# Optimization experiments

Hardware: AMD Instinct MI355X
Metric: run time of the kernel (lower is better)

Reference implementation:

```python
import jax, jax.numpy as jnp
import numpy as np

TAU = 0.1  # temperature (registered buffer, non-trainable)
EPS = 1e-12  # F.normalize eps


def setup_inputs() -> dict:
    key = jax.random.key(0)
    k1, k2 = jax.random.split(key)
    B, C = 4096, 512
    z1 = jax.random.normal(k1, (B, C), dtype=jnp.float32)
    z2 = jax.random.normal(k2, (B, C), dtype=jnp.float32)
    return {"z1": z1, "z2": z2}


def _l2_normalize(x):
    # matches F.normalize(p=2, dim=1): x / max(||x||, eps)
    n = jnp.sqrt(jnp.sum(x * x, axis=1, keepdims=True))
    return x / jnp.maximum(n, EPS)


def reference(z1, z2):
    B = z1.shape[0]
    N = 2 * B
    z = jnp.concatenate([_l2_normalize(z1), _l2_normalize(z2)], axis=0)  # [2B, C]
    # cosine similarity of unit vectors == dot product -> single GEMM
    S = jnp.exp((z @ z.T) / TAU)  # [2B, 2B]
    rows = jnp.arange(N)
    pos_cols = (rows + B) % N  # mask[r, c]=1 iff r == (c+B) mod 2B  <=> c == (r+B) mod 2B
    positive = S[rows, pos_cols]                 # [2B]
    # negatives = row sum over ~mask; note the original INCLUDES the diagonal
    negative = jnp.sum(S, axis=1) - positive     # [2B]
    pairs_loss = -jnp.log(positive / negative)   # [2B]
    loss = pairs_loss.reshape(2, B).sum(axis=0) / N  # [B]
    return loss.mean()  # reduce=True
```

## Files before the change

### kernel.cpp

```cpp
#include <hip/hip_runtime.h>
#include <hip/hip_bf16.h>


#define BDIM 4096
#define CDIM 512
#define NROWS 8192
#define NTILE 32
#define NKT 8
#define NBLK 576

typedef __attribute__((ext_vector_type(4))) float f32x4;
typedef __attribute__((ext_vector_type(8))) short bf16x8;

#define AS1 __attribute__((address_space(1)))
#define AS3 __attribute__((address_space(3)))

__device__ __forceinline__ unsigned short f2bf_rne(float x) {
    unsigned u = __float_as_uint(x);
    u += 0x7fffu + ((u >> 16) & 1u);
    return (unsigned short)(u >> 16);
}

__global__ __launch_bounds__(256) void normalize_kernel(
    const float* __restrict__ z1, const float* __restrict__ z2,
    unsigned short* __restrict__ zb, float* __restrict__ pos10,
    float* __restrict__ rowsum, float* __restrict__ out) {
    if (blockIdx.x == 0) {
#pragma unroll
        for (int i = 0; i < NROWS / 256; ++i) rowsum[i * 256 + threadIdx.x] = 0.f;
        if (threadIdx.x == 0) out[0] = 0.f;
    }
    const int w = threadIdx.x >> 6, lane = threadIdx.x & 63;
    const int r = blockIdx.x * 4 + w;
    const float4* p1 = (const float4*)(z1 + (size_t)r * CDIM);
    const float4* p2 = (const float4*)(z2 + (size_t)r * CDIM);
    float4 a0 = p1[lane], a1 = p1[64 + lane];
    float4 b0 = p2[lane], b1 = p2[64 + lane];
    float s1 = a0.x * a0.x + a0.y * a0.y + a0.z * a0.z + a0.w * a0.w +
               a1.x * a1.x + a1.y * a1.y + a1.z * a1.z + a1.w * a1.w;
    float s2 = b0.x * b0.x + b0.y * b0.y + b0.z * b0.z + b0.w * b0.w +
               b1.x * b1.x + b1.y * b1.y + b1.z * b1.z + b1.w * b1.w;
    float d = a0.x * b0.x + a0.y * b0.y + a0.z * b0.z + a0.w * b0.w +
              a1.x * b1.x + a1.y * b1.y + a1.z * b1.z + a1.w * b1.w;
#pragma unroll
    for (int m = 1; m < 64; m <<= 1) {
        s1 += __shfl_xor(s1, m, 64);
        s2 += __shfl_xor(s2, m, 64);
        d += __shfl_xor(d, m, 64);
    }
    const float n1 = fmaxf(sqrtf(s1), 1e-12f);
    const float n2 = fmaxf(sqrtf(s2), 1e-12f);
    const float i1 = 1.0f / n1, i2 = 1.0f / n2;
    ushort4 o;
    ushort4* q1 = (ushort4*)(zb + (size_t)r * CDIM);
    ushort4* q2 = (ushort4*)(zb + (size_t)(r + BDIM) * CDIM);
    o.x = f2bf_rne(a0.x * i1); o.y = f2bf_rne(a0.y * i1);
    o.z = f2bf_rne(a0.z * i1); o.w = f2bf_rne(a0.w * i1);
    q1[lane] = o;
    o.x = f2bf_rne(a1.x * i1); o.y = f2bf_rne(a1.y * i1);
    o.z = f2bf_rne(a1.z * i1); o.w = f2bf_rne(a1.w * i1);
    q1[64 + lane] = o;
    o.x = f2bf_rne(b0.x * i2); o.y = f2bf_rne(b0.y * i2);
    o.z = f2bf_rne(b0.z * i2); o.w = f2bf_rne(b0.w * i2);
    q2[lane] = o;
    o.x = f2bf_rne(b1.x * i2); o.y = f2bf_rne(b1.y * i2);
    o.z = f2bf_rne(b1.z * i2); o.w = f2bf_rne(b1.w * i2);
    q2[64 + lane] = o;
    if (lane == 0) pos10[r] = (d / (n1 * n2)) * 10.0f;
}

__global__ __launch_bounds__(512, 2) void simgemm_kernel(
    const unsigned short* __restrict__ Z, float* __restrict__ rowsum) {
    __shared__ unsigned short lds[2][4][128 * 64];

    const int t = threadIdx.x;
    const int lane = t & 63, w = t >> 6;
    const int wr = w >> 2, wc = w & 3;
    const int srow = t >> 3;
    const int scolb = (((t & 7) ^ ((t >> 3) & 7)) << 4);
    const char* Zb = (const char*)Z;
    const float SC = 14.4269504088896340736f;
    const int g = lane >> 4;
    const int arow = lane & 15;
    const int klo = (lane >> 4) << 4;
    const int swz = (lane & 7) << 4;
    const int bid = blockIdx.x;

    if (bid < 512) {
        const int fid = (bid & 7) * 64 + (bid >> 3);
        int by = 0, rem = fid;
        while (true) {
            const int cnt = (NTILE - by) - (by <= 15 ? 1 : 0);
            if (rem < cnt) break;
            rem -= cnt; ++by;
        }
        int bx = by + rem;
        if (by <= 15 && bx >= 31 - by) ++bx;
        const bool diag = (bx == by);

        f32x4 acc[8][4] = {};
        const size_t apan = ((size_t)(by * 256) << 10);
        const size_t bpan = ((size_t)(bx * 256) << 10);

#define STG(T, J)                                                                \
    {                                                                            \
        const size_t pb_ = ((J) < 2 ? apan : bpan);                              \
        const char* g0_ = Zb + pb_ +                                             \
            ((size_t)((((J) & 1) * 128) + srow) << 10) + ((T) * 128) + scolb;    \
        char* d0_ = (char*)&lds[(T) & 1][J][0] + w * 1024;                       \
        __builtin_amdgcn_global_load_lds((const AS1 void*)g0_,                   \
                                         (AS3 void*)d0_, 16, 0, 0);              \
        __builtin_amdgcn_global_load_lds((const AS1 void*)(g0_ + (64 << 10)),    \
                                         (AS3 void*)(d0_ + 8192), 16, 0, 0);     \
    }

        STG(0, 2); STG(0, 3); STG(0, 0); STG(0, 1); STG(1, 2); STG(1, 0);
        asm volatile("s_waitcnt vmcnt(4)\n\ts_barrier" ::: "memory");

        const int brow0 = (wc & 1) * 64;
#pragma unroll
        for (int T = 0; T < NKT; ++T) {
            const int buf = T & 1;
            const char* Ab = (const char*)&lds[buf][wr][0];
            const char* Bb = (const char*)&lds[buf][2 + (wc >> 1)][0];
            if (T >= 1) {
                if (T < NKT - 1)
                    asm volatile("s_waitcnt vmcnt(4)\n\ts_barrier" ::: "memory");
                else
                    asm volatile("s_waitcnt vmcnt(0)\n\ts_barrier" ::: "memory");
            }

            bf16x8 af[4][2], bf[4][2];

#pragma unroll
            for (int mi = 0; mi < 4; ++mi)
#pragma unroll
                for (int kk = 0; kk < 2; ++kk)
                    af[mi][kk] = *(const bf16x8*)(Ab + (mi * 16 + arow) * 128 +
                                                  ((kk * 64 + klo) ^ swz));
#pragma unroll
            for (int ni = 0; ni < 2; ++ni)
#pragma unroll
                for (int kk = 0; kk < 2; ++kk)
                    bf[ni][kk] = *(const bf16x8*)(Bb + (brow0 + ni * 16 + arow) * 128 +
                                                  ((kk * 64 + klo) ^ swz));
            if (T + 1 < NKT) STG(T + 1, 3);
            asm volatile("s_barrier" ::: "memory");
            __builtin_amdgcn_s_setprio(1);
#pragma unroll
            for (int mi = 0; mi < 4; ++mi)
#pragma unroll
                for (int ni = 0; ni < 2; ++ni)
#pragma unroll
                    for (int kk = 0; kk < 2; ++kk)
                        acc[mi][ni] = __builtin_amdgcn_mfma_f32_16x16x32_bf16(
                            af[mi][kk], bf[ni][kk], acc[mi][ni], 0, 0, 0);
            __builtin_amdgcn_s_setprio(0);
            asm volatile("s_waitcnt lgkmcnt(0)\n\ts_barrier" ::: "memory");

#pragma unroll
            for (int ni = 2; ni < 4; ++ni)
#pragma unroll
                for (int kk = 0; kk < 2; ++kk)
                    bf[ni][kk] = *(const bf16x8*)(Bb + (brow0 + ni * 16 + arow) * 128 +
                                                  ((kk * 64 + klo) ^ swz));
            if (T + 1 < NKT) STG(T + 1, 1);
            asm volatile("s_barrier" ::: "memory");
            __builtin_amdgcn_s_setprio(1);
#pragma unroll
            for (int mi = 0; mi < 4; ++mi)
#pragma unroll
                for (int ni = 2; ni < 4; ++ni)
#pragma unroll
                    for (int kk = 0; kk < 2; ++kk)
                        acc[mi][ni] = __builtin_amdgcn_mfma_f32_16x16x32_bf16(
                            af[mi][kk], bf[ni][kk], acc[mi][ni], 0, 0, 0);
            __builtin_amdgcn_s_setprio(0);
            asm volatile("s_waitcnt lgkmcnt(0)\n\ts_barrier" ::: "memory");

#pragma unroll
            for (int mi = 0; mi < 4; ++mi)
#pragma unroll
                for (int kk = 0; kk < 2; ++kk)
                    af[mi][kk] = *(const bf16x8*)(Ab + ((mi + 4) * 16 + arow) * 128 +
                                                  ((kk * 64 + klo) ^ swz));
            if (T + 2 < NKT) STG(T + 2, 2);
            asm volatile("s_barrier" ::: "memory");
            __builtin_amdgcn_s_setprio(1);
#pragma unroll
            for (int mi = 0; mi < 4; ++mi)
#pragma unroll
                for (int ni = 0; ni < 2; ++ni)
#pragma unroll
                    for (int kk = 0; kk < 2; ++kk)
                        acc[mi + 4][ni] = __builtin_amdgcn_mfma_f32_16x16x32_bf16(
                            af[mi][kk], bf[ni][kk], acc[mi + 4][ni], 0, 0, 0);
            __builtin_amdgcn_s_setprio(0);
            asm volatile("s_waitcnt lgkmcnt(0)\n\ts_barrier" ::: "memory");

            if (T + 2 < NKT) STG(T + 2, 0);
            asm volatile("s_barrier" ::: "memory");
            __builtin_amdgcn_s_setprio(1);
#pragma unroll
            for (int mi = 0; mi < 4; ++mi)
#pragma unroll
                for (int ni = 2; ni < 4; ++ni)
#pragma unroll
                    for (int kk = 0; kk < 2; ++kk)
                        acc[mi + 4][ni] = __builtin_amdgcn_mfma_f32_16x16x32_bf16(
                            af[mi][kk], bf[ni][kk], acc[mi + 4][ni], 0, 0, 0);
            __builtin_amdgcn_s_setprio(0);
            asm volatile("s_waitcnt lgkmcnt(0)\n\ts_barrier" ::: "memory");
        }
#undef STG

        float cs[4] = {0.f, 0.f, 0.f, 0.f};
#pragma unroll
        for (int mi = 0; mi < 8; ++mi) {
            float rs0 = 0.f, rs1 = 0.f, rs2 = 0.f, rs3 = 0.f;
#pragma unroll
            for (int ni = 0; ni < 4; ++ni) {
                f32x4 a = acc[mi][ni];
                const float e0 = exp2f(a[0] * SC);
                const float e1 = exp2f(a[1] * SC);
                const float e2 = exp2f(a[2] * SC);
                const float e3 = exp2f(a[3] * SC);
                rs0 += e0; rs1 += e1; rs2 += e2; rs3 += e3;
                cs[ni] += (e0 + e1) + (e2 + e3);
            }
#pragma unroll
            for (int m = 1; m < 16; m <<= 1) {
                rs0 += __shfl_xor(rs0, m, 64);
                rs1 += __shfl_xor(rs1, m, 64);
                rs2 += __shfl_xor(rs2, m, 64);
                rs3 += __shfl_xor(rs3, m, 64);
            }
            if ((lane & 15) == 0) {
                const int rbase = by * 256 + wr * 128 + mi * 16 + g * 4;
                atomicAdd(&rowsum[rbase + 0], rs0);
                atomicAdd(&rowsum[rbase + 1], rs1);
                atomicAdd(&rowsum[rbase + 2], rs2);
                atomicAdd(&rowsum[rbase + 3], rs3);
            }
        }
        if (!diag) {
#pragma unroll
            for (int ni = 0; ni < 4; ++ni) {
                float c = cs[ni];
                c += __shfl_xor(c, 16, 64);
                c += __shfl_xor(c, 32, 64);
                if (lane < 16)
                    atomicAdd(&rowsum[bx * 256 + wc * 64 + ni * 16 + lane], c);
            }
        }
    } else {
        const int qi = bid - 512;
        const int by = qi >> 2, bx = 31 - (qi >> 2), cq = qi & 3;
        const size_t apan = ((size_t)(by * 256) << 10);
        const size_t bq = ((size_t)(bx * 256 + cq * 64) << 10);

        f32x4 accq[8] = {};

#define GLD(gp, dp) __builtin_amdgcn_global_load_lds((const AS1 void*)(gp), (AS3 void*)(dp), 16, 0, 0)
#define STGQ(T, d)                                                               \
    {                                                                            \
        _Pragma("unroll") for (int J_ = 0; J_ < 2; ++J_) {                       \
            const char* g0_ = Zb + apan +                                        \
                ((size_t)(J_ * 128 + srow) << 10) + ((T) << 7) + scolb;          \
            char* d0_ = (char*)&lds[d][J_][0] + w * 1024;                        \
            GLD(g0_, d0_);                                                       \
            GLD(g0_ + (64 << 10), d0_ + 8192);                                   \
        }                                                                        \
        GLD(Zb + bq + ((size_t)srow << 10) + ((T) << 7) + scolb,                 \
            (char*)&lds[d][2][0] + w * 1024);                                    \
    }

        STGQ(0, 0);
        __syncthreads();
#pragma unroll
        for (int T = 0; T < NKT; ++T) {
            const int d = T & 1;
            if (T < NKT - 1) STGQ(T + 1, d ^ 1);
            const char* Aw = (const char*)&lds[d][wr][0];
            const char* Bq = (const char*)&lds[d][2][0];
#pragma unroll
            for (int kk = 0; kk < 2; ++kk) {
                const int koff = (kk * 64 + klo) ^ swz;
                bf16x8 bfq = *(const bf16x8*)(Bq + (wc * 16 + arow) * 128 + koff);
#pragma unroll
                for (int mi = 0; mi < 8; ++mi) {
                    bf16x8 afm = *(const bf16x8*)(Aw + (mi * 16 + arow) * 128 + koff);
                    accq[mi] = __builtin_amdgcn_mfma_f32_16x16x32_bf16(
                        afm, bfq, accq[mi], 0, 0, 0);
                }
            }
            __syncthreads();
        }
#undef STGQ
#undef GLD

        float cs = 0.f;
#pragma unroll
        for (int mi = 0; mi < 8; ++mi) {
            f32x4 a = accq[mi];
            const float e0 = exp2f(a[0] * SC);
            const float e1 = exp2f(a[1] * SC);
            const float e2 = exp2f(a[2] * SC);
            const float e3 = exp2f(a[3] * SC);
            float rs0 = e0, rs1 = e1, rs2 = e2, rs3 = e3;
            cs += (e0 + e1) + (e2 + e3);
#pragma unroll
            for (int m = 1; m < 16; m <<= 1) {
                rs0 += __shfl_xor(rs0, m, 64);
                rs1 += __shfl_xor(rs1, m, 64);
                rs2 += __shfl_xor(rs2, m, 64);
                rs3 += __shfl_xor(rs3, m, 64);
            }
            if ((lane & 15) == 0) {
                const int rbase = by * 256 + wr * 128 + mi * 16 + g * 4;
                atomicAdd(&rowsum[rbase + 0], rs0);
                atomicAdd(&rowsum[rbase + 1], rs1);
                atomicAdd(&rowsum[rbase + 2], rs2);
                atomicAdd(&rowsum[rbase + 3], rs3);
            }
        }
        cs += __shfl_xor(cs, 16, 64);
        cs += __shfl_xor(cs, 32, 64);
        if (lane < 16)
            atomicAdd(&rowsum[bx * 256 + cq * 64 + wc * 16 + lane], cs);
    }
}

__global__ __launch_bounds__(256) void finalize_kernel(
    const float* __restrict__ rowsum, const float* __restrict__ pos10,
    float* __restrict__ out) {
    __shared__ float sm[4];
    const int w = threadIdx.x >> 6, lane = threadIdx.x & 63;
    const int r = blockIdx.x * 256 + threadIdx.x;
    const float p10 = pos10[r];
    const float pos = expf(p10);
    float l = (logf(rowsum[r] - pos) - p10) +
              (logf(rowsum[r + BDIM] - pos) - p10);
#pragma unroll
    for (int m = 1; m < 64; m <<= 1) l += __shfl_xor(l, m, 64);
    if (lane == 0) sm[w] = l;
    __syncthreads();
    if (threadIdx.x == 0) {
        const float tot = sm[0] + sm[1] + sm[2] + sm[3];
        atomicAdd(out, tot * (1.0f / ((float)NROWS * (float)BDIM)));
    }
}

extern "C" void kernel_launch(void* const* d_in, const int* in_sizes, int n_in,
                              void* d_out, int out_size, void* d_ws, size_t ws_size,
                              hipStream_t stream) {
    const float* z1 = (const float*)d_in[0];
    const float* z2 = (const float*)d_in[1];
    float* out = (float*)d_out;
    unsigned short* zb = (unsigned short*)d_ws;
    float* rowsum = (float*)((char*)d_ws + (size_t)NROWS * CDIM * 2);
    float* pos10 = rowsum + NROWS;

    normalize_kernel<<<BDIM / 4, 256, 0, stream>>>(z1, z2, zb, pos10, rowsum, out);
    simgemm_kernel<<<NBLK, 512, 0, stream>>>(zb, rowsum);
    finalize_kernel<<<BDIM / 256, 256, 0, stream>>>(rowsum, pos10, out);
}
```

Before: 139.0 us.

## Make similarity GEMM persistent with atomic job queue and fuse finalize

The similarity GEMM kernel becomes persistent: 256 blocks pull tile jobs from a global atomic ticket counter instead of one block per tile. The finalize step is folded into the GEMM kernel, where the last block to finish, found with a second ticket counter, computes the loss, so one kernel launch goes away. The aim is better load balance across the uneven full-tile and quarter-tile jobs and less launch overhead. In exchange it drops the previous block-id swizzle that grouped tiles for cache locality. With launch bounds lowered to one block per CU, fewer blocks are resident per CU, which may hurt latency hiding.

```diff
diff --git a/kernel.cpp b/kernel.cpp
--- a/kernel.cpp
+++ b/kernel.cpp
@@ -7,7 +7,8 @@
 #define NROWS 8192
 #define NTILE 32
 #define NKT 8
-#define NBLK 576
+#define NJOBS 576
+#define NPBLK 256
 
 typedef __attribute__((ext_vector_type(4))) float f32x4;
 typedef __attribute__((ext_vector_type(8))) short bf16x8;
@@ -24,11 +25,12 @@
 __global__ __launch_bounds__(256) void normalize_kernel(
     const float* __restrict__ z1, const float* __restrict__ z2,
     unsigned short* __restrict__ zb, float* __restrict__ pos10,
-    float* __restrict__ rowsum, float* __restrict__ out) {
+    float* __restrict__ rowsum, float* __restrict__ out,
+    unsigned* __restrict__ tickets) {
     if (blockIdx.x == 0) {
 #pragma unroll
         for (int i = 0; i < NROWS / 256; ++i) rowsum[i * 256 + threadIdx.x] = 0.f;
-        if (threadIdx.x == 0) out[0] = 0.f;
+        if (threadIdx.x == 0) { out[0] = 0.f; tickets[0] = 0u; tickets[1] = 0u; }
     }
     const int w = threadIdx.x >> 6, lane = threadIdx.x & 63;
     const int r = blockIdx.x * 4 + w;
@@ -69,9 +71,14 @@
     if (lane == 0) pos10[r] = (d / (n1 * n2)) * 10.0f;
 }
 
-__global__ __launch_bounds__(512, 2) void simgemm_kernel(
-    const unsigned short* __restrict__ Z, float* __restrict__ rowsum) {
+__global__ __launch_bounds__(512, 1) void simgemm_kernel(
+    const unsigned short* __restrict__ Z, float* __restrict__ rowsum,
+    const float* __restrict__ pos10, float* __restrict__ out,
+    unsigned* __restrict__ tickets) {
     __shared__ unsigned short lds[2][4][128 * 64];
+    __shared__ int sm_job;
+    __shared__ float redsm[8];
+    __shared__ unsigned lastsm;
 
     const int t = threadIdx.x;
     const int lane = t & 63, w = t >> 6;
@@ -84,23 +91,27 @@
     const int arow = lane & 15;
     const int klo = (lane >> 4) << 4;
     const int swz = (lane & 7) << 4;
-    const int bid = blockIdx.x;
-
-    if (bid < 512) {
-        const int fid = (bid & 7) * 64 + (bid >> 3);
-        int by = 0, rem = fid;
-        while (true) {
-            const int cnt = (NTILE - by) - (by <= 15 ? 1 : 0);
-            if (rem < cnt) break;
-            rem -= cnt; ++by;
-        }
-        int bx = by + rem;
-        if (by <= 15 && bx >= 31 - by) ++bx;
-        const bool diag = (bx == by);
-
-        f32x4 acc[8][4] = {};
-        const size_t apan = ((size_t)(by * 256) << 10);
-        const size_t bpan = ((size_t)(bx * 256) << 10);
+
+    for (;;) {
+        if (t == 0) sm_job = (int)atomicAdd(&tickets[0], 1u);
+        __syncthreads();
+        const int job = sm_job;
+        if (job >= NJOBS) break;
+
+        if (job < 512) {
+            int by = 0, rem = job;
+            while (true) {
+                const int cnt = (NTILE - by) - (by <= 15 ? 1 : 0);
+                if (rem < cnt) break;
+                rem -= cnt; ++by;
+            }
+            int bx = by + rem;
+            if (by <= 15 && bx >= 31 - by) ++bx;
+            const bool diag = (bx == by);
+
+            f32x4 acc[8][4] = {};
+            const size_t apan = ((size_t)(by * 256) << 10);
+            const size_t bpan = ((size_t)(bx * 256) << 10);
 
 #define STG(T, J)                                                                \
     {                                                                            \
@@ -114,152 +125,152 @@
                                          (AS3 void*)(d0_ + 8192), 16, 0, 0);     \
     }
 
-        STG(0, 2); STG(0, 3); STG(0, 0); STG(0, 1); STG(1, 2); STG(1, 0);
-        asm volatile("s_waitcnt vmcnt(4)\n\ts_barrier" ::: "memory");
-
-        const int brow0 = (wc & 1) * 64;
-#pragma unroll
-        for (int T = 0; T < NKT; ++T) {
-            const int buf = T & 1;
-            const char* Ab = (const char*)&lds[buf][wr][0];
-            const char* Bb = (const char*)&lds[buf][2 + (wc >> 1)][0];
-            if (T >= 1) {
-                if (T < NKT - 1)
-                    asm volatile("s_waitcnt vmcnt(4)\n\ts_barrier" ::: "memory");
-                else
-                    asm volatile("s_waitcnt vmcnt(0)\n\ts_barrier" ::: "memory");
-            }
-
-            bf16x8 af[4][2], bf[4][2];
-
-#pragma unroll
-            for (int mi = 0; mi < 4; ++mi)
-#pragma unroll
-                for (int kk = 0; kk < 2; ++kk)
-                    af[mi][kk] = *(const bf16x8*)(Ab + (mi * 16 + arow) * 128 +
-                                                  ((kk * 64 + klo) ^ swz));
-#pragma unroll
-            for (int ni = 0; ni < 2; ++ni)
-#pragma unroll
-                for (int kk = 0; kk < 2; ++kk)
-                    bf[ni][kk] = *(const bf16x8*)(Bb + (brow0 + ni * 16 + arow) * 128 +
-                                                  ((kk * 64 + klo) ^ swz));
-            if (T + 1 < NKT) STG(T + 1, 3);
-            asm volatile("s_barrier" ::: "memory");
-            __builtin_amdgcn_s_setprio(1);
-#pragma unroll
-            for (int mi = 0; mi < 4; ++mi)
+            STG(0, 2); STG(0, 3); STG(0, 0); STG(0, 1); STG(1, 2); STG(1, 0);
+            asm volatile("s_waitcnt vmcnt(4)\n\ts_barrier" ::: "memory");
+
+            const int brow0 = (wc & 1) * 64;
+#pragma unroll
+            for (int T = 0; T < NKT; ++T) {
+                const int buf = T & 1;
+                const char* Ab = (const char*)&lds[buf][wr][0];
+                const char* Bb = (const char*)&lds[buf][2 + (wc >> 1)][0];
+                if (T >= 1) {
+                    if (T < NKT - 1)
+                        asm volatile("s_waitcnt vmcnt(4)\n\ts_barrier" ::: "memory");
+                    else
+                        asm volatile("s_waitcnt vmcnt(0)\n\ts_barrier" ::: "memory");
+                }
+
+                bf16x8 af[4][2], bf[4][2];
+
+#pragma unroll
+                for (int mi = 0; mi < 4; ++mi)
+#pragma unroll
+                    for (int kk = 0; kk < 2; ++kk)
+                        af[mi][kk] = *(const bf16x8*)(Ab + (mi * 16 + arow) * 128 +
+                                                      ((kk * 64 + klo) ^ swz));
 #pragma unroll
                 for (int ni = 0; ni < 2; ++ni)
 #pragma unroll
                     for (int kk = 0; kk < 2; ++kk)
-                        acc[mi][ni] = __builtin_amdgcn_mfma_f32_16x16x32_bf16(
-                            af[mi][kk], bf[ni][kk], acc[mi][ni], 0, 0, 0);
-            __builtin_amdgcn_s_setprio(0);
-            asm volatile("s_waitcnt lgkmcnt(0)\n\ts_barrier" ::: "memory");
-
-#pragma unroll
-            for (int ni = 2; ni < 4; ++ni)
-#pragma unroll
-                for (int kk = 0; kk < 2; ++kk)
-                    bf[ni][kk] = *(const bf16x8*)(Bb + (brow0 + ni * 16 + arow) * 128 +
-                                                  ((kk * 64 + klo) ^ swz));
-            if (T + 1 < NKT) STG(T + 1, 1);
-            asm volatile("s_barrier" ::: "memory");
-            __builtin_amdgcn_s_setprio(1);
-#pragma unroll
-            for (int mi = 0; mi < 4; ++mi)
+                        bf[ni][kk] = *(const bf16x8*)(Bb + (brow0 + ni * 16 + arow) * 128 +
+                                                      ((kk * 64 + klo) ^ swz));
+                if (T + 1 < NKT) STG(T + 1, 3);
+                asm volatile("s_barrier" ::: "memory");
+                __builtin_amdgcn_s_setprio(1);
+#pragma unroll
+                for (int mi = 0; mi < 4; ++mi)
+#pragma unroll
+                    for (int ni = 0; ni < 2; ++ni)
+#pragma unroll
+                        for (int kk = 0; kk < 2; ++kk)
+                            acc[mi][ni] = __builtin_amdgcn_mfma_f32_16x16x32_bf16(
+                                af[mi][kk], bf[ni][kk], acc[mi][ni], 0, 0, 0);
+                __builtin_amdgcn_s_setprio(0);
+                asm volatile("s_waitcnt lgkmcnt(0)\n\ts_barrier" ::: "memory");
+
 #pragma unroll
                 for (int ni = 2; ni < 4; ++ni)
 #pragma unroll
                     for (int kk = 0; kk < 2; ++kk)
-                        acc[mi][ni] = __builtin_amdgcn_mfma_f32_16x16x32_bf16(
-                            af[mi][kk], bf[ni][kk], acc[mi][ni], 0, 0, 0);
-            __builtin_amdgcn_s_setprio(0);
-            asm volatile("s_waitcnt lgkmcnt(0)\n\ts_barrier" ::: "memory");
-
-#pragma unroll
-            for (int mi = 0; mi < 4; ++mi)
-#pragma unroll
-                for (int kk = 0; kk < 2; ++kk)
-                    af[mi][kk] = *(const bf16x8*)(Ab + ((mi + 4) * 16 + arow) * 128 +
-                                                  ((kk * 64 + klo) ^ swz));
-            if (T + 2 < NKT) STG(T + 2, 2);
-            asm volatile("s_barrier" ::: "memory");
-            __builtin_amdgcn_s_setprio(1);
-#pragma unroll
-            for (int mi = 0; mi < 4; ++mi)
-#pragma unroll
-                for (int ni = 0; ni < 2; ++ni)
+                        bf[ni][kk] = *(const bf16x8*)(Bb + (brow0 + ni * 16 + arow) * 128 +
+                                                      ((kk * 64 + klo) ^ swz));
+                if (T + 1 < NKT) STG(T + 1, 1);
+                asm volatile("s_barrier" ::: "memory");
+                __builtin_amdgcn_s_setprio(1);
+#pragma unroll
+                for (int mi = 0; mi < 4; ++mi)
+#pragma unroll
+                    for (int ni = 2; ni < 4; ++ni)
+#pragma unroll
+                        for (int kk = 0; kk < 2; ++kk)
+                            acc[mi][ni] = __builtin_amdgcn_mfma_f32_16x16x32_bf16(
+                                af[mi][kk], bf[ni][kk], acc[mi][ni], 0, 0, 0);
+                __builtin_amdgcn_s_setprio(0);
+                asm volatile("s_waitcnt lgkmcnt(0)\n\ts_barrier" ::: "memory");
+
+#pragma unroll
+                for (int mi = 0; mi < 4; ++mi)
 #pragma unroll
                     for (int kk = 0; kk < 2; ++kk)
-                        acc[mi + 4][ni] = __builtin_amdgcn_mfma_f32_16x16x32_bf16(
-                            af[mi][kk], bf[ni][kk], acc[mi + 4][ni], 0, 0, 0);
-            __builtin_amdgcn_s_setprio(0);
-            asm volatile("s_waitcnt lgkmcnt(0)\n\ts_barrier" ::: "memory");
-
-            if (T + 2 < NKT) STG(T + 2, 0);
-            asm volatile("s_barrier" ::: "memory");
-            __builtin_amdgcn_s_setprio(1);
-#pragma unroll
-            for (int mi = 0; mi < 4; ++mi)
-#pragma unroll
-                for (int ni = 2; ni < 4; ++ni)
-#pragma unroll
-                    for (int kk = 0; kk < 2; ++kk)
-                        acc[mi + 4][ni] = __builtin_amdgcn_mfma_f32_16x16x32_bf16(
-                            af[mi][kk], bf[ni][kk], acc[mi + 4][ni], 0, 0, 0);
-            __builtin_amdgcn_s_setprio(0);
-            asm volatile("s_waitcnt lgkmcnt(0)\n\ts_barrier" ::: "memory");
-        }
+                        af[mi][kk] = *(const bf16x8*)(Ab + ((mi + 4) * 16 + arow) * 128 +
+                                                      ((kk * 64 + klo) ^ swz));
+                if (T + 2 < NKT) STG(T + 2, 2);
+                asm volatile("s_barrier" ::: "memory");
+                __builtin_amdgcn_s_setprio(1);
+#pragma unroll
+                for (int mi = 0; mi < 4; ++mi)
+#pragma unroll
+                    for (int ni = 0; ni < 2; ++ni)
+#pragma unroll
+                        for (int kk = 0; kk < 2; ++kk)
+                            acc[mi + 4][ni] = __builtin_amdgcn_mfma_f32_16x16x32_bf16(
+                                af[mi][kk], bf[ni][kk], acc[mi + 4][ni], 0, 0, 0);
+                __builtin_amdgcn_s_setprio(0);
+                asm volatile("s_waitcnt lgkmcnt(0)\n\ts_barrier" ::: "memory");
+
+                if (T + 2 < NKT) STG(T + 2, 0);
+                asm volatile("s_barrier" ::: "memory");
+                __builtin_amdgcn_s_setprio(1);
+#pragma unroll
+                for (int mi = 0; mi < 4; ++mi)
+#pragma unroll
+                    for (int ni = 2; ni < 4; ++ni)
+#pragma unroll
+                        for (int kk = 0; kk < 2; ++kk)
+                            acc[mi + 4][ni] = __builtin_amdgcn_mfma_f32_16x16x32_bf16(
+                                af[mi][kk], bf[ni][kk], acc[mi + 4][ni], 0, 0, 0);
+                __builtin_amdgcn_s_setprio(0);
+                asm volatile("s_waitcnt lgkmcnt(0)\n\ts_barrier" ::: "memory");
+            }
 #undef STG
 
-        float cs[4] = {0.f, 0.f, 0.f, 0.f};
-#pragma unroll
-        for (int mi = 0; mi < 8; ++mi) {
-            float rs0 = 0.f, rs1 = 0.f, rs2 = 0.f, rs3 = 0.f;
-#pragma unroll
-            for (int ni = 0; ni < 4; ++ni) {
-                f32x4 a = acc[mi][ni];
-                const float e0 = exp2f(a[0] * SC);
-                const float e1 = exp2f(a[1] * SC);
-                const float e2 = exp2f(a[2] * SC);
-                const float e3 = exp2f(a[3] * SC);
-                rs0 += e0; rs1 += e1; rs2 += e2; rs3 += e3;
-                cs[ni] += (e0 + e1) + (e2 + e3);
-            }
-#pragma unroll
-            for (int m = 1; m < 16; m <<= 1) {
-                rs0 += __shfl_xor(rs0, m, 64);
-                rs1 += __shfl_xor(rs1, m, 64);
-                rs2 += __shfl_xor(rs2, m, 64);
-                rs3 += __shfl_xor(rs3, m, 64);
-            }
-            if ((lane & 15) == 0) {
-                const int rbase = by * 256 + wr * 128 + mi * 16 + g * 4;
-                atomicAdd(&rowsum[rbase + 0], rs0);
-                atomicAdd(&rowsum[rbase + 1], rs1);
-                atomicAdd(&rowsum[rbase + 2], rs2);
-                atomicAdd(&rowsum[rbase + 3], rs3);
-            }
-        }
-        if (!diag) {
-#pragma unroll
-            for (int ni = 0; ni < 4; ++ni) {
-                float c = cs[ni];
-                c += __shfl_xor(c, 16, 64);
-                c += __shfl_xor(c, 32, 64);
-                if (lane < 16)
-                    atomicAdd(&rowsum[bx * 256 + wc * 64 + ni * 16 + lane], c);
-            }
-        }
-    } else {
-        const int qi = bid - 512;
-        const int by = qi >> 2, bx = 31 - (qi >> 2), cq = qi & 3;
-        const size_t apan = ((size_t)(by * 256) << 10);
-        const size_t bq = ((size_t)(bx * 256 + cq * 64) << 10);
-
-        f32x4 accq[8] = {};
+            float cs[4] = {0.f, 0.f, 0.f, 0.f};
+#pragma unroll
+            for (int mi = 0; mi < 8; ++mi) {
+                float rs0 = 0.f, rs1 = 0.f, rs2 = 0.f, rs3 = 0.f;
+#pragma unroll
+                for (int ni = 0; ni < 4; ++ni) {
+                    f32x4 a = acc[mi][ni];
+                    const float e0 = exp2f(a[0] * SC);
+                    const float e1 = exp2f(a[1] * SC);
+                    const float e2 = exp2f(a[2] * SC);
+                    const float e3 = exp2f(a[3] * SC);
+                    rs0 += e0; rs1 += e1; rs2 += e2; rs3 += e3;
+                    cs[ni] += (e0 + e1) + (e2 + e3);
+                }
+#pragma unroll
+                for (int m = 1; m < 16; m <<= 1) {
+                    rs0 += __shfl_xor(rs0, m, 64);
+                    rs1 += __shfl_xor(rs1, m, 64);
+                    rs2 += __shfl_xor(rs2, m, 64);
+                    rs3 += __shfl_xor(rs3, m, 64);
+                }
+                if ((lane & 15) == 0) {
+                    const int rbase = by * 256 + wr * 128 + mi * 16 + g * 4;
+                    atomicAdd(&rowsum[rbase + 0], rs0);
+                    atomicAdd(&rowsum[rbase + 1], rs1);
+                    atomicAdd(&rowsum[rbase + 2], rs2);
+                    atomicAdd(&rowsum[rbase + 3], rs3);
+                }
+            }
+            if (!diag) {
+#pragma unroll
+                for (int ni = 0; ni < 4; ++ni) {
+                    float c = cs[ni];
+                    c += __shfl_xor(c, 16, 64);
+                    c += __shfl_xor(c, 32, 64);
+                    if (lane < 16)
+                        atomicAdd(&rowsum[bx * 256 + wc * 64 + ni * 16 + lane], c);
+                }
+            }
+        } else {
+            const int qi = job - 512;
+            const int by = qi >> 2, bx = 31 - (qi >> 2), cq = qi & 3;
+            const size_t apan = ((size_t)(by * 256) << 10);
+            const size_t bq = ((size_t)(bx * 256 + cq * 64) << 10);
+
+            f32x4 accq[8] = {};
 
 #define GLD(gp, dp) __builtin_amdgcn_global_load_lds((const AS1 void*)(gp), (AS3 void*)(dp), 16, 0, 0)
 #define STGQ(T, d)                                                               \
@@ -275,79 +286,84 @@
             (char*)&lds[d][2][0] + w * 1024);                                    \
     }
 
-        STGQ(0, 0);
-        __syncthreads();
-#pragma unroll
-        for (int T = 0; T < NKT; ++T) {
-            const int d = T & 1;
-            if (T < NKT - 1) STGQ(T + 1, d ^ 1);
-            const char* Aw = (const char*)&lds[d][wr][0];
-            const char* Bq = (const char*)&lds[d][2][0];
-#pragma unroll
-            for (int kk = 0; kk < 2; ++kk) {
-                const int koff = (kk * 64 + klo) ^ swz;
-                bf16x8 bfq = *(const bf16x8*)(Bq + (wc * 16 + arow) * 128 + koff);
-#pragma unroll
-                for (int mi = 0; mi < 8; ++mi) {
-                    bf16x8 afm = *(const bf16x8*)(Aw + (mi * 16 + arow) * 128 + koff);
-                    accq[mi] = __builtin_amdgcn_mfma_f32_16x16x32_bf16(
-                        afm, bfq, accq[mi], 0, 0, 0);
-                }
-            }
+            STGQ(0, 0);
             __syncthreads();
-        }
+#pragma unroll
+            for (int T = 0; T < NKT; ++T) {
+                const int d = T & 1;
+                if (T < NKT - 1) STGQ(T + 1, d ^ 1);
+                const char* Aw = (const char*)&lds[d][wr][0];
+                const char* Bq = (const char*)&lds[d][2][0];
+#pragma unroll
+                for (int kk = 0; kk < 2; ++kk) {
+                    const int koff = (kk * 64 + klo) ^ swz;
+                    bf16x8 bfq = *(const bf16x8*)(Bq + (wc * 16 + arow) * 128 + koff);
+#pragma unroll
+                    for (int mi = 0; mi < 8; ++mi) {
+                        bf16x8 afm = *(const bf16x8*)(Aw + (mi * 16 + arow) * 128 + koff);
+                        accq[mi] = __builtin_amdgcn_mfma_f32_16x16x32_bf16(
+                            afm, bfq, accq[mi], 0, 0, 0);
+                    }
+                }
+                __syncthreads();
+            }
 #undef STGQ
 #undef GLD
 
-        float cs = 0.f;
-#pragma unroll
-        for (int mi = 0; mi < 8; ++mi) {
-            f32x4 a = accq[mi];
-            const float e0 = exp2f(a[0] * SC);
-            const float e1 = exp2f(a[1] * SC);
-            const float e2 = exp2f(a[2] * SC);
-            const float e3 = exp2f(a[3] * SC);
-            float rs0 = e0, rs1 = e1, rs2 = e2, rs3 = e3;
-            cs += (e0 + e1) + (e2 + e3);
-#pragma unroll
-            for (int m = 1; m < 16; m <<= 1) {
-                rs0 += __shfl_xor(rs0, m, 64);
-                rs1 += __shfl_xor(rs1, m, 64);
-                rs2 += __shfl_xor(rs2, m, 64);
-                rs3 += __shfl_xor(rs3, m, 64);
-            }
-            if ((lane & 15) == 0) {
-                const int rbase = by * 256 + wr * 128 + mi * 16 + g * 4;
-                atomicAdd(&rowsum[rbase + 0], rs0);
-                atomicAdd(&rowsum[rbase + 1], rs1);
-                atomicAdd(&rowsum[rbase + 2], rs2);
-                atomicAdd(&rowsum[rbase + 3], rs3);
-            }
+            float cs = 0.f;
+#pragma unroll
+            for (int mi = 0; mi < 8; ++mi) {
+                f32x4 a = accq[mi];
+                const float e0 = exp2f(a[0] * SC);
+                const float e1 = exp2f(a[1] * SC);
+                const float e2 = exp2f(a[2] * SC);
+                const float e3 = exp2f(a[3] * SC);
+                float rs0 = e0, rs1 = e1, rs2 = e2, rs3 = e3;
+                cs += (e0 + e1) + (e2 + e3);
+#pragma unroll
+                for (int m = 1; m < 16; m <<= 1) {
+                    rs0 += __shfl_xor(rs0, m, 64);
+                    rs1 += __shfl_xor(rs1, m, 64);
+                    rs2 += __shfl_xor(rs2, m, 64);
+                    rs3 += __shfl_xor(rs3, m, 64);
+                }
+                if ((lane & 15) == 0) {
+                    const int rbase = by * 256 + wr * 128 + mi * 16 + g * 4;
+                    atomicAdd(&rowsum[rbase + 0], rs0);
+                    atomicAdd(&rowsum[rbase + 1], rs1);
+                    atomicAdd(&rowsum[rbase + 2], rs2);
+                    atomicAdd(&rowsum[rbase + 3], rs3);
+                }
+            }
+            cs += __shfl_xor(cs, 16, 64);
+            cs += __shfl_xor(cs, 32, 64);
+            if (lane < 16)
+                atomicAdd(&rowsum[bx * 256 + cq * 64 + wc * 16 + lane], cs);
         }
-        cs += __shfl_xor(cs, 16, 64);
-        cs += __shfl_xor(cs, 32, 64);
-        if (lane < 16)
-            atomicAdd(&rowsum[bx * 256 + cq * 64 + wc * 16 + lane], cs);
-    }
-}
-
-__global__ __launch_bounds__(256) void finalize_kernel(
-    const float* __restrict__ rowsum, const float* __restrict__ pos10,
-    float* __restrict__ out) {
-    __shared__ float sm[4];
-    const int w = threadIdx.x >> 6, lane = threadIdx.x & 63;
-    const int r = blockIdx.x * 256 + threadIdx.x;
-    const float p10 = pos10[r];
-    const float pos = expf(p10);
-    float l = (logf(rowsum[r] - pos) - p10) +
-              (logf(rowsum[r + BDIM] - pos) - p10);
-#pragma unroll
-    for (int m = 1; m < 64; m <<= 1) l += __shfl_xor(l, m, 64);
-    if (lane == 0) sm[w] = l;
+    }
+
+    __threadfence();
+    if (t == 0) lastsm = (atomicAdd(&tickets[1], 1u) == (unsigned)(NPBLK - 1)) ? 1u : 0u;
     __syncthreads();
-    if (threadIdx.x == 0) {
-        const float tot = sm[0] + sm[1] + sm[2] + sm[3];
-        atomicAdd(out, tot * (1.0f / ((float)NROWS * (float)BDIM)));
+    if (lastsm) {
+        float l = 0.f;
+        for (int r = t; r < BDIM; r += 512) {
+            const float rs1 = atomicAdd(&rowsum[r], 0.f);
+            const float rs2 = atomicAdd(&rowsum[r + BDIM], 0.f);
+            const float p10 = pos10[r];
+            const float pos = expf(p10);
+            l += (logf(rs1 - pos) - p10) + (logf(rs2 - pos) - p10);
+        }
+#pragma unroll
+        for (int m = 1; m < 64; m <<= 1) l += __shfl_xor(l, m, 64);
+        if (lane == 0) redsm[w] = l;
+        __syncthreads();
+        if (t == 0) {
+            float tot = 0.f;
+#pragma unroll
+            for (int i = 0; i < 8; ++i) tot += redsm[i];
+            out[0] = tot * (1.0f / ((float)NROWS * (float)BDIM));
+        }
     }
 }
 
@@ -360,8 +376,8 @@
     unsigned short* zb = (unsigned short*)d_ws;
     float* rowsum = (float*)((char*)d_ws + (size_t)NROWS * CDIM * 2);
     float* pos10 = rowsum + NROWS;
-
-    normalize_kernel<<<BDIM / 4, 256, 0, stream>>>(z1, z2, zb, pos10, rowsum, out);
-    simgemm_kernel<<<NBLK, 512, 0, stream>>>(zb, rowsum);
-    finalize_kernel<<<BDIM / 256, 256, 0, stream>>>(rowsum, pos10, out);
+    unsigned* tickets = (unsigned*)(pos10 + BDIM);
+
+    normalize_kernel<<<BDIM / 4, 256, 0, stream>>>(z1, z2, zb, pos10, rowsum, out, tickets);
+    simgemm_kernel<<<NPBLK, 512, 0, stream>>>(zb, rowsum, pos10, out, tickets);
 }
```

After: 183.6 us. 32.0% more time.
